# Kernel tuning notes

Measured on AMD Instinct MI355X. Metric: run time of the kernel, lower is better.

The kernel has to match this reference:

```python
import jax, jax.numpy as jnp
import numpy as np

B, L, V, E, D, NH, HD, NL = 4, 2048, 32000, 300, 128, 4, 128, 3
D2 = NH * HD  # 512
W = 3  # ring window size (unfold_size)
EPS = 1e-5


def setup_inputs() -> dict:
    key = jax.random.key(0)
    ks = jax.random.split(key, 16)
    s = 0.02
    w = lambda k, shape: (jax.random.normal(k, shape, jnp.float32) * s)
    inp = {
        "tokens": jax.random.randint(ks[0], (B, L), 0, V),
        "mask": jax.random.randint(ks[1], (B, L), 0, 2).astype(jnp.int32),
        "emb_table": w(ks[2], (V, E)),
        "proj_w": w(ks[3], (D, E)),
        "proj_b": jnp.zeros((D,), jnp.float32),
        "ng": jnp.ones((NL, D), jnp.float32),
        "nb": jnp.zeros((NL, D), jnp.float32),
        "rq_w": w(ks[4], (NL, D2, D)), "rq_b": jnp.zeros((NL, D2), jnp.float32),
        "rk_w": w(ks[5], (NL, D2, D)), "rk_b": jnp.zeros((NL, D2), jnp.float32),
        "rv_w": w(ks[6], (NL, D2, D)), "rv_b": jnp.zeros((NL, D2), jnp.float32),
        "ro_w": w(ks[7], (NL, D, D2)), "ro_b": jnp.zeros((NL, D), jnp.float32),
        "sq_w": w(ks[8], (NL, D2, D)), "sq_b": jnp.zeros((NL, D2), jnp.float32),
        "sk_w": w(ks[9], (NL, D2, D)), "sk_b": jnp.zeros((NL, D2), jnp.float32),
        "sv_w": w(ks[10], (NL, D2, D)), "sv_b": jnp.zeros((NL, D2), jnp.float32),
        "so_w": w(ks[11], (NL, D, D2)), "so_b": jnp.zeros((NL, D), jnp.float32),
    }
    return inp


def _layernorm(x, g, b):
    mu = x.mean(-1, keepdims=True)
    var = x.var(-1, keepdims=True)
    return (x - mu) / jnp.sqrt(var + EPS) * g + b


def reference(tokens, mask, emb_table, proj_w, proj_b, ng, nb,
              rq_w, rq_b, rk_w, rk_b, rv_w, rv_b, ro_w, ro_b,
              sq_w, sq_b, sk_w, sk_b, sv_w, sv_b, so_w, so_b):
    b, l = tokens.shape
    pad = (mask == 0)                                        # [B,L] True at padding
    smask = jnp.concatenate([jnp.zeros((b, 1), bool), pad], axis=1)  # [B,L+1]
    x = emb_table[tokens] @ proj_w.T + proj_b                # [B,L,D]
    nodes = x
    relay = x.mean(axis=1)                                   # [B,D]
    r_embs = x                                               # fixed original embeddings
    scale = 1.0 / np.sqrt(HD).astype(np.float32)
    for i in range(NL):
        nx = _layernorm(nodes, ng[i], nb[i])
        # ----- MSA1: ring (windowed) attention + relay extras -----
        q = (nx @ rq_w[i].T + rq_b[i]).reshape(b, l, NH, HD)
        k = (nx @ rk_w[i].T + rk_b[i]).reshape(b, l, NH, HD)
        v = (nx @ rv_w[i].T + rv_b[i]).reshape(b, l, NH, HD)
        relay_bc = jnp.broadcast_to(relay[:, None, :], (b, l, D))
        ax = jnp.stack([r_embs, relay_bc], axis=2)           # [B,L,2,D]
        ak = (ax @ rk_w[i].T + rk_b[i]).reshape(b, l, 2, NH, HD)
        av = (ax @ rv_w[i].T + rv_b[i]).reshape(b, l, 2, NH, HD)
        kp = jnp.pad(k, ((0, 0), (1, 1), (0, 0), (0, 0)))    # zero pad like F.unfold
        vp = jnp.pad(v, ((0, 0), (1, 1), (0, 0), (0, 0)))
        kw = jnp.stack([kp[:, u:u + l] for u in range(W)], axis=2)  # [B,L,3,NH,HD]
        vw = jnp.stack([vp[:, u:u + l] for u in range(W)], axis=2)
        kall = jnp.concatenate([kw, ak], axis=2)             # [B,L,5,NH,HD]
        vall = jnp.concatenate([vw, av], axis=2)
        scores = jnp.einsum('blnh,blunh->blun', q, kall) * scale
        alphas = jax.nn.softmax(scores, axis=2)
        att = jnp.einsum('blun,blunh->blnh', alphas, vall).reshape(b, l, D2)
        nodes = nodes + jax.nn.leaky_relu(att @ ro_w[i].T + ro_b[i])
        # ----- MSA2: relay (global) attention over [relay; nodes] -----
        y = jnp.concatenate([relay[:, None, :], nodes], axis=1)      # [B,L+1,D]
        sq = (relay @ sq_w[i].T + sq_b[i]).reshape(b, NH, HD)
        sk = (y @ sk_w[i].T + sk_b[i]).reshape(b, l + 1, NH, HD)
        sv = (y @ sv_w[i].T + sv_b[i]).reshape(b, l + 1, NH, HD)
        pre = jnp.einsum('bnh,blnh->bnl', sq, sk) * scale            # [B,NH,L+1]
        pre = jnp.where(smask[:, None, :], -jnp.inf, pre)
        al = jax.nn.softmax(pre, axis=2)
        satt = jnp.einsum('bnl,blnh->bnh', al, sv).reshape(b, D2)
        relay = jax.nn.leaky_relu(satt @ so_w[i].T + so_b[i])
        nodes = jnp.where(pad[:, :, None], 0.0, nodes)
    return relay  # a_v: [B, d_model] (use_attention=False path)
```

## Files before the change

### kernel.cpp

```cpp
#include <hip/hip_runtime.h>
#include <hip/hip_bf16.h>

constexpr int B = 4, L = 2048, E = 300, D = 128, NH = 4, HD = 128, NL = 3, D2 = 512;
constexpr float EPS = 1e-5f;
constexpr float SCALE = 0.08838834764831843f;
constexpr int NCH = 64;

typedef unsigned int uint_t;
typedef unsigned short u16;
typedef short bf16x8 __attribute__((ext_vector_type(8)));
typedef float f32x4 __attribute__((ext_vector_type(4)));

__device__ __forceinline__ u16 f2bf(float f) {
  union { float f; uint_t i; } x; x.f = f;
  uint_t r = x.i + 0x7fffu + ((x.i >> 16) & 1u);
  return (u16)(r >> 16);
}
__device__ __forceinline__ uint_t packbf(float a, float b) {
  return (uint_t)f2bf(a) | ((uint_t)f2bf(b) << 16);
}
__device__ __forceinline__ float2 bf2x2(uint_t u) {
  union { uint_t i; float f; } a, b;
  a.i = (u & 0xffffu) << 16; b.i = u & 0xffff0000u;
  return make_float2(a.f, b.f);
}
struct f8 { float v[8]; };
__device__ __forceinline__ f8 unpack8(uint4 u) {
  f8 r;
  float2 a = bf2x2(u.x); r.v[0] = a.x; r.v[1] = a.y;
  float2 b = bf2x2(u.y); r.v[2] = b.x; r.v[3] = b.y;
  float2 c = bf2x2(u.z); r.v[4] = c.x; r.v[5] = c.y;
  float2 d = bf2x2(u.w); r.v[6] = d.x; r.v[7] = d.y;
  return r;
}

struct WCArgs { const float* s[4]; u16* d[4]; };

struct GDesc { const u16* A; const u16* W; const float* bias; u16* outb; };
struct GArgs { GDesc d[5]; };
struct PArgs {
  int mode;
  const float* rel_in;
  const float* pm; const float* ps; const float* pw;
  const float* uprev; const float* cvprev;
  const float* svw; const float* svb;
  const float* sow; const float* sob;
  float* rel_out;
  const float* rkw; const float* rkb;
  const float* rvw; const float* rvb;
  const float* sqw; const float* sqb;
  const float* skw; const float* skb;
  float* relay_k; float* relay_v;
  float* u; float* cvec;
};
constexpr int NPROJ = 24;

__global__ __launch_bounds__(256) void gemm_qkv(GArgs ga, PArgs pa, int N) {
  int bid = blockIdx.x;
  int t = threadIdx.x;
  if (bid < NPROJ) {
    __shared__ float rel[D];
    __shared__ float sql2[2][HD];
    __shared__ float credp[4];
    __shared__ float wsum2[NH][D];
    __shared__ float satts[D2];
    __shared__ float ecs2[256];
    int b = bid / 6, j = bid % 6;
    int wv = t >> 6, lane = t & 63;
    if (pa.mode) {
      if (t < D) rel[t] = pa.rel_in[(size_t)b * D + t];
      __syncthreads();
      float2 uu = ((const float2*)(pa.uprev + ((size_t)b * NH + wv) * D))[lane];
      float2 rr = ((const float2*)rel)[lane];
      float pdot = uu.x * rr.x + uu.y * rr.y;
#pragma unroll
      for (int o = 1; o < 64; o <<= 1) pdot += __shfl_xor(pdot, o, 64);
      float s0 = pdot + pa.cvprev[b * NH + wv];
      int bn = b * NH + wv;
      float pmv = pa.pm[bn * NCH + lane];
      float m = fmaxf(pmv, s0);
#pragma unroll
      for (int o = 1; o < 64; o <<= 1) m = fmaxf(m, __shfl_xor(m, o, 64));
      float ec = expf(pmv - m);
      ecs2[wv * 64 + lane] = ec;
      float sc = pa.ps[bn * NCH + lane] * ec;
#pragma unroll
      for (int o = 1; o < 64; o <<= 1) sc += __shfl_xor(sc, o, 64);
      float e0 = expf(s0 - m);
      float invS = 1.0f / (e0 + sc);
      float2 a;
      a.x = e0 * rel[lane * 2]; a.y = e0 * rel[lane * 2 + 1];
      const float* pwb = pa.pw + (size_t)bn * NCH * D;
#pragma unroll 8
      for (int c = 0; c < NCH; c++) {
        float2 pw2 = ((const float2*)(pwb + (size_t)c * D))[lane];
        float e = ecs2[wv * 64 + c];
        a.x += e * pw2.x; a.y += e * pw2.y;
      }
      wsum2[wv][lane * 2] = a.x * invS;
      wsum2[wv][lane * 2 + 1] = a.y * invS;
      __syncthreads();
#pragma unroll
      for (int pp = 0; pp < 2; pp++) {
        int nh = pp * 256 + t, n = nh >> 7;
        float acc = pa.svb[nh];
        const float4* wp = (const float4*)(pa.svw + (size_t)nh * D);
        const float4* wl = (const float4*)wsum2[n];
#pragma unroll 8
        for (int dd = 0; dd < D / 4; dd++) {
          float4 x = wl[dd], y = wp[dd];
          acc += x.x * y.x + x.y * y.y + x.z * y.z + x.w * y.w;
        }
        satts[nh] = acc;
      }
      __syncthreads();
      {
        int part = t >> 7, col = t & 127;
        float acc = 0.f;
        const float4* wp = (const float4*)(pa.sow + (size_t)col * D2 + part * 256);
        const float4* a4 = (const float4*)(satts + part * 256);
#pragma unroll 8
        for (int jj = 0; jj < 64; jj++) {
          float4 x = a4[jj], y = wp[jj];
          acc += x.x * y.x + x.y * y.y + x.z * y.z + x.w * y.w;
        }
        ecs2[part * 128 + col] = acc;
      }
      __syncthreads();
      if (t < D) {
        float av = pa.sob[t] + ecs2[t] + ecs2[128 + t];
        av = (av > 0.f) ? av : 0.01f * av;
        rel[t] = av;
        pa.rel_out[(size_t)b * D + t] = av;
      }
      __syncthreads();
    } else {
      if (t < D) rel[t] = pa.rel_in[(size_t)b * D + t];
      __syncthreads();
    }
    const float4* r4 = (const float4*)rel;
    if (j < 4) {
      int which = j >> 1;
      int n = (j & 1) * 256 + t;
      const float* W = which ? pa.rvw : pa.rkw;
      float acc = (which ? pa.rvb : pa.rkb)[n];
      const float4* w4 = (const float4*)(W + (size_t)n * D);
#pragma unroll 8
      for (int i = 0; i < D / 4; i++) {
        float4 w = w4[i], r = r4[i];
        acc += w.x * r.x + w.y * r.y + w.z * r.z + w.w * r.w;
      }
      (which ? pa.relay_v : pa.relay_k)[(size_t)b * D2 + n] = acc;
    } else {
      int hh = t >> 7, th = t & 127;
      int n = (j - 4) * 2 + hh;
      int nh = n * HD + th;
      float acc = pa.sqb[nh];
      const float4* w4 = (const float4*)(pa.sqw + (size_t)nh * D);
#pragma unroll 8
      for (int i = 0; i < D / 4; i++) {
        float4 w = w4[i], r = r4[i];
        acc += w.x * r.x + w.y * r.y + w.z * r.z + w.w * r.w;
      }
      sql2[hh][th] = acc;
      __syncthreads();
      float cp = acc * pa.skb[nh];
#pragma unroll
      for (int o = 1; o < 64; o <<= 1) cp += __shfl_xor(cp, o, 64);
      if ((t & 63) == 0) credp[t >> 6] = cp;
      float a0 = 0.f, a1 = 0.f, a2 = 0.f, a3 = 0.f;
      const float* wp = pa.skw + (size_t)(n * HD) * D + th;
      for (int hx = 0; hx < HD; hx += 4) {
        a0 += sql2[hh][hx] * wp[(size_t)hx * D];
        a1 += sql2[hh][hx + 1] * wp[(size_t)(hx + 1) * D];
        a2 += sql2[hh][hx + 2] * wp[(size_t)(hx + 2) * D];
        a3 += sql2[hh][hx + 3] * wp[(size_t)(hx + 3) * D];
      }
      pa.u[((size_t)b * NH + n) * D + th] = (a0 + a1 + a2 + a3) * SCALE;
      __syncthreads();
      if (th == 0) pa.cvec[b * NH + n] = (credp[2 * hh] + credp[2 * hh + 1]) * SCALE;
    }
    return;
  }
  __shared__ u16 As[128][136];
  __shared__ u16 Ws[128][136];
  int g = bid - NPROJ;
  int grp = g >> 8;
  int bm = (g & 255) >> 2, bn = g & 3;
  const int di0 = grp ? 3 : 0;
  const int ntens = grp ? 2 : 3;
  const int rowA = bm * 128, rowW = bn * 128;

  const int r = t >> 1, c0 = (t & 1) * 64;
  const int wid = t >> 6;
  const int wm = (wid & 1) * 64, wn = (wid >> 1) * 64;
  const int lr = t & 15, quad = (t >> 4) & 3;

  {
    const u16* Arow = ga.d[di0].A + (size_t)(rowA + r) * 128;
    uint4 av_[8];
#pragma unroll
    for (int i = 0; i < 8; i++) av_[i] = *(const uint4*)(Arow + c0 + i * 8);
#pragma unroll
    for (int i = 0; i < 8; i++) *(uint4*)&As[r][c0 + i * 8] = av_[i];
  }
  for (int ti = 0; ti < ntens; ti++) {
    GDesc d = ga.d[di0 + ti];
    {
      const u16* Wrow = d.W + (size_t)(rowW + r) * 128;
      uint4 wv_[8];
#pragma unroll
      for (int i = 0; i < 8; i++) wv_[i] = *(const uint4*)(Wrow + c0 + i * 8);
#pragma unroll
      for (int i = 0; i < 8; i++) *(uint4*)&Ws[r][c0 + i * 8] = wv_[i];
    }
    __syncthreads();
    f32x4 acc[4][4];
#pragma unroll
    for (int i = 0; i < 4; i++)
#pragma unroll
      for (int j = 0; j < 4; j++)
        acc[i][j] = (f32x4){0.f, 0.f, 0.f, 0.f};
#pragma unroll
    for (int ks = 0; ks < 4; ks++) {
      bf16x8 af[4], bfr[4];
#pragma unroll
      for (int mt = 0; mt < 4; mt++)
        af[mt] = *(const bf16x8*)&As[wm + mt * 16 + lr][ks * 32 + quad * 8];
#pragma unroll
      for (int nt = 0; nt < 4; nt++)
        bfr[nt] = *(const bf16x8*)&Ws[wn + nt * 16 + lr][ks * 32 + quad * 8];
#pragma unroll
      for (int mt = 0; mt < 4; mt++)
#pragma unroll
        for (int nt = 0; nt < 4; nt++)
          acc[mt][nt] = __builtin_amdgcn_mfma_f32_16x16x32_bf16(af[mt], bfr[nt], acc[mt][nt], 0, 0, 0);
    }
    __syncthreads();
#pragma unroll
    for (int nt = 0; nt < 4; nt++) {
      int colL = wn + nt * 16 + lr;
      float bv = d.bias[rowW + colL];
#pragma unroll
      for (int mt = 0; mt < 4; mt++) {
#pragma unroll
        for (int rr = 0; rr < 4; rr++) {
          int rowL = wm + mt * 16 + quad * 4 + rr;
          Ws[rowL][colL] = f2bf(acc[mt][nt][rr] + bv);
        }
      }
    }
    __syncthreads();
#pragma unroll
    for (int rep = 0; rep < 8; rep++) {
      int lin = rep * 256 + t;
      int rowL = lin >> 4, colL = (lin & 15) * 8;
      uint4 v = *(const uint4*)&Ws[rowL][colL];
      *(uint4*)&d.outb[(size_t)(rowA + rowL) * N + rowW + colL] = v;
    }
    __syncthreads();
  }
}

__global__ __launch_bounds__(256) void gemm_embed_ln(
    WCArgs wa,
    const float* __restrict__ emb, const float* __restrict__ W,
    const float* __restrict__ bias, const int* __restrict__ gather,
    const float* __restrict__ lng, const float* __restrict__ lnb,
    float* __restrict__ nodes, u16* __restrict__ xb, u16* __restrict__ nxb,
    float* __restrict__ relay) {
  int bid = blockIdx.x;
  int t = threadIdx.x;
  if (bid >= 128) {
    int cb = bid - 128;
    int ti = cb / 192, xi = cb - ti * 192;
    const float* s = wa.s[ti]; u16* dd = wa.d[ti];
    int i = (xi * 256 + t) * 4;
    float4 f = *(const float4*)(s + i);
    *(uint2*)(dd + i) = make_uint2(packbf(f.x, f.y), packbf(f.z, f.w));
    return;
  }
  __shared__ u16 As[64][72];
  __shared__ u16 Ws[128][72];
  __shared__ float C[64][132];
  __shared__ float gb[2][D];
  __shared__ float lmu[64], lrs[64];
  int bm = bid;
  const int rowA0 = bm * 64;

  f32x4 acc[2][4];
#pragma unroll
  for (int i = 0; i < 2; i++)
#pragma unroll
    for (int j = 0; j < 4; j++)
      acc[i][j] = (f32x4){0.f, 0.f, 0.f, 0.f};

  const int wid = t >> 6;
  const int wm = (wid & 1) * 32, wn = (wid >> 1) * 64;
  const int lr = t & 15, quad = (t >> 4) & 3;
  const int ra = t >> 2, ca = (t & 3) * 16;
  const int rw = t >> 1, cw = (t & 1) * 32;

  if (t < D) { gb[0][t] = lng[t]; gb[1][t] = lnb[t]; }

  const float* Arow = emb + (size_t)gather[rowA0 + ra] * E;
  const float* Wrow = W + (size_t)rw * E;

  for (int kt = 0; kt < E; kt += 64) {
    __syncthreads();
    bool full = (kt + 64 <= E);
#pragma unroll
    for (int ch = 0; ch < 4; ch++) {
      int c = kt + ca + ch * 4;
      float4 fa;
      if (full) fa = *(const float4*)(Arow + c);
      else {
        fa.x = (c + 0 < E) ? Arow[c + 0] : 0.f;
        fa.y = (c + 1 < E) ? Arow[c + 1] : 0.f;
        fa.z = (c + 2 < E) ? Arow[c + 2] : 0.f;
        fa.w = (c + 3 < E) ? Arow[c + 3] : 0.f;
      }
      *(uint2*)&As[ra][ca + ch * 4] = make_uint2(packbf(fa.x, fa.y), packbf(fa.z, fa.w));
    }
#pragma unroll
    for (int ch = 0; ch < 8; ch++) {
      int c = kt + cw + ch * 4;
      float4 fw;
      if (full) fw = *(const float4*)(Wrow + c);
      else {
        fw.x = (c + 0 < E) ? Wrow[c + 0] : 0.f;
        fw.y = (c + 1 < E) ? Wrow[c + 1] : 0.f;
        fw.z = (c + 2 < E) ? Wrow[c + 2] : 0.f;
        fw.w = (c + 3 < E) ? Wrow[c + 3] : 0.f;
      }
      *(uint2*)&Ws[rw][cw + ch * 4] = make_uint2(packbf(fw.x, fw.y), packbf(fw.z, fw.w));
    }
    __syncthreads();
#pragma unroll
    for (int ks = 0; ks < 2; ks++) {
      bf16x8 af[2], bfr[4];
#pragma unroll
      for (int mt = 0; mt < 2; mt++)
        af[mt] = *(const bf16x8*)&As[wm + mt * 16 + lr][ks * 32 + quad * 8];
#pragma unroll
      for (int nt = 0; nt < 4; nt++)
        bfr[nt] = *(const bf16x8*)&Ws[wn + nt * 16 + lr][ks * 32 + quad * 8];
#pragma unroll
      for (int mt = 0; mt < 2; mt++)
#pragma unroll
        for (int nt = 0; nt < 4; nt++)
          acc[mt][nt] = __builtin_amdgcn_mfma_f32_16x16x32_bf16(af[mt], bfr[nt], acc[mt][nt], 0, 0, 0);
    }
  }
#pragma unroll
  for (int nt = 0; nt < 4; nt++) {
    int col = wn + nt * 16 + lr;
    float bv = bias[col];
#pragma unroll
    for (int mt = 0; mt < 2; mt++) {
#pragma unroll
      for (int rr = 0; rr < 4; rr++) {
        int row = wm + mt * 16 + quad * 4 + rr;
        C[row][col] = acc[mt][nt][rr] + bv;
      }
    }
  }
  __syncthreads();
  if (t < 64) {
    float s = 0.f, s2 = 0.f;
#pragma unroll 16
    for (int j = 0; j < D; j++) { float v = C[t][j]; s += v; s2 += v * v; }
    float mu = s * (1.0f / D);
    float var = s2 * (1.0f / D) - mu * mu;
    lmu[t] = mu; lrs[t] = rsqrtf(var + EPS);
  }
  __syncthreads();
#pragma unroll
  for (int rep = 0; rep < 8; rep++) {
    int lin = rep * 1024 + t * 4;
    int row = lin >> 7, col = lin & 127;
    float4 v = *(const float4*)&C[row][col];
    size_t g = (size_t)(rowA0 + row) * D + col;
    *(float4*)&nodes[g] = v;
    *(uint2*)&xb[g] = make_uint2(packbf(v.x, v.y), packbf(v.z, v.w));
    float mu = lmu[row], rs = lrs[row];
    float o0 = (v.x - mu) * rs * gb[0][col] + gb[1][col];
    float o1 = (v.y - mu) * rs * gb[0][col + 1] + gb[1][col + 1];
    float o2 = (v.z - mu) * rs * gb[0][col + 2] + gb[1][col + 2];
    float o3 = (v.w - mu) * rs * gb[0][col + 3] + gb[1][col + 3];
    *(uint2*)&nxb[g] = make_uint2(packbf(o0, o1), packbf(o2, o3));
  }
  if (t < D) {
    int b = rowA0 >> 11;
    float s = 0.f;
#pragma unroll 16
    for (int r2 = 0; r2 < 64; r2++) s += C[r2][t];
    atomicAdd(&relay[b * D + t], s * (1.0f / L));
  }
}

__global__ __launch_bounds__(512) void attn_ro_ln(
    const u16* __restrict__ q, const u16* __restrict__ k, const u16* __restrict__ v,
    const u16* __restrict__ akr, const u16* __restrict__ avr,
    const float* __restrict__ rkvec, const float* __restrict__ rvvec,
    const u16* __restrict__ W,
    const float* __restrict__ bias,
    const int* __restrict__ mask,
    const float* __restrict__ lng, const float* __restrict__ lnb,
    const float* __restrict__ uvec, const float* __restrict__ cvec,
    float* __restrict__ nodes, u16* __restrict__ nxb,
    float* __restrict__ pm, float* __restrict__ ps, float* __restrict__ pw,
    int do_ln) {
  __shared__ u16 att[32][520];
  __shared__ u16 Ws[128][136];
  __shared__ float C[32][132];
  __shared__ float gb[2][D];
  __shared__ float lmu[32], lrs[32];
  __shared__ float usv[NH][D];
  __shared__ float cv2[NH];
  __shared__ float scs[NH][32];
  __shared__ float esr[NH][32];
  int t = threadIdx.x;
  int bm = blockIdx.x;
  const int rowA0 = bm * 32;
  const int b4 = rowA0 >> 11;
  const int chunk = (rowA0 >> 5) & 63;
  const int wid = t >> 6, lane = t & 63;

  if (do_ln && t < D) { gb[0][t] = lng[t]; gb[1][t] = lnb[t]; }
  usv[t >> 7][t & 127] = uvec[(size_t)b4 * NH * D + t];
  if (t < NH) cv2[t] = cvec[b4 * NH + t];

  {
    size_t rb = (size_t)b4 * D2 + lane * 8;
    float4 rk0 = *(const float4*)(rkvec + rb), rk1 = *(const float4*)(rkvec + rb + 4);
    float4 rv0 = *(const float4*)(rvvec + rb), rv1 = *(const float4*)(rvvec + rb + 4);
    f8 krel, vrel;
    krel.v[0] = rk0.x; krel.v[1] = rk0.y; krel.v[2] = rk0.z; krel.v[3] = rk0.w;
    krel.v[4] = rk1.x; krel.v[5] = rk1.y; krel.v[6] = rk1.z; krel.v[7] = rk1.w;
    vrel.v[0] = rv0.x; vrel.v[1] = rv0.y; vrel.v[2] = rv0.z; vrel.v[3] = rv0.w;
    vrel.v[4] = rv1.x; vrel.v[5] = rv1.y; vrel.v[6] = rv1.z; vrel.v[7] = rv1.w;
#pragma unroll
    for (int i = 0; i < 4; i++) {
      int rr_ = wid * 4 + i;
      int gr = rowA0 + rr_;
      int l = gr & (L - 1);
      size_t rowoff = (size_t)gr * D2 + lane * 8;
      uint4 qd = *(const uint4*)(q + rowoff);
      uint4 kd[4], vd[4];
#pragma unroll
      for (int u2 = 0; u2 < 3; u2++) {
        int ll = l + u2 - 1;
        bool ok = (ll >= 0 && ll < L);
        size_t off = rowoff + (size_t)(u2 - 1) * (size_t)D2;
        if (ok) { kd[u2] = *(const uint4*)(k + off); vd[u2] = *(const uint4*)(v + off); }
        else { kd[u2] = make_uint4(0, 0, 0, 0); vd[u2] = make_uint4(0, 0, 0, 0); }
      }
      kd[3] = *(const uint4*)(akr + rowoff);
      vd[3] = *(const uint4*)(avr + rowoff);
      f8 qf = unpack8(qd);
      f8 kf[5], vf[5];
#pragma unroll
      for (int u2 = 0; u2 < 4; u2++) { kf[u2] = unpack8(kd[u2]); vf[u2] = unpack8(vd[u2]); }
      kf[4] = krel; vf[4] = vrel;
      float s[5];
#pragma unroll
      for (int u2 = 0; u2 < 5; u2++) {
        float p = 0.f;
#pragma unroll
        for (int j = 0; j < 8; j++) p += qf.v[j] * kf[u2].v[j];
#pragma unroll
        for (int o = 1; o < 16; o <<= 1) p += __shfl_xor(p, o, 64);
        s[u2] = p * SCALE;
      }
      float m = s[0];
#pragma unroll
      for (int u2 = 1; u2 < 5; u2++) m = fmaxf(m, s[u2]);
      float e[5], sum = 0.f;
#pragma unroll
      for (int u2 = 0; u2 < 5; u2++) { e[u2] = expf(s[u2] - m); sum += e[u2]; }
      float inv = 1.0f / sum;
      float o8[8];
#pragma unroll
      for (int j = 0; j < 8; j++) {
        float a = 0.f;
#pragma unroll
        for (int u2 = 0; u2 < 5; u2++) a += e[u2] * vf[u2].v[j];
        o8[j] = a * inv;
      }
      uint4 od;
      od.x = packbf(o8[0], o8[1]); od.y = packbf(o8[2], o8[3]);
      od.z = packbf(o8[4], o8[5]); od.w = packbf(o8[6], o8[7]);
      *(uint4*)&att[rr_][lane * 8] = od;
    }
  }
  __syncthreads();

  f32x4 acc[2];
  acc[0] = (f32x4){0.f, 0.f, 0.f, 0.f};
  acc[1] = (f32x4){0.f, 0.f, 0.f, 0.f};
  const int wm = (wid & 1) * 16, wn = (wid >> 1) * 32;
  const int lr = t & 15, quad = (t >> 4) & 3;
  const int rw = t >> 2, cw = (t & 3) * 32;
  const u16* Wrow = W + (size_t)rw * 512;
  for (int kt = 0; kt < 512; kt += 128) {
    uint4 w0 = *(const uint4*)(Wrow + kt + cw);
    uint4 w1 = *(const uint4*)(Wrow + kt + cw + 8);
    uint4 w2 = *(const uint4*)(Wrow + kt + cw + 16);
    uint4 w3 = *(const uint4*)(Wrow + kt + cw + 24);
    __syncthreads();
    *(uint4*)&Ws[rw][cw] = w0; *(uint4*)&Ws[rw][cw + 8] = w1;
    *(uint4*)&Ws[rw][cw + 16] = w2; *(uint4*)&Ws[rw][cw + 24] = w3;
    __syncthreads();
#pragma unroll
    for (int ks = 0; ks < 4; ks++) {
      bf16x8 af = *(const bf16x8*)&att[wm + lr][kt + ks * 32 + quad * 8];
#pragma unroll
      for (int nt = 0; nt < 2; nt++) {
        bf16x8 bfr = *(const bf16x8*)&Ws[wn + nt * 16 + lr][ks * 32 + quad * 8];
        acc[nt] = __builtin_amdgcn_mfma_f32_16x16x32_bf16(af, bfr, acc[nt], 0, 0, 0);
      }
    }
  }
  __syncthreads();
#pragma unroll
  for (int nt = 0; nt < 2; nt++) {
    int col = wn + nt * 16 + lr;
    float bv = bias[col];
#pragma unroll
    for (int rr = 0; rr < 4; rr++) {
      int row = wm + quad * 4 + rr;
      float vv = acc[nt][rr] + bv;
      vv = (vv > 0.f) ? vv : 0.01f * vv;
      vv += nodes[(size_t)(rowA0 + row) * D + col];
      if (mask[rowA0 + row] == 0) vv = 0.f;
      C[row][col] = vv;
    }
  }
  __syncthreads();
  if (t < 32) {
    float s = 0.f, s2 = 0.f;
#pragma unroll 16
    for (int j = 0; j < D; j++) { float vv = C[t][j]; s += vv; s2 += vv * vv; }
    float mu = s * (1.0f / D);
    float var = s2 * (1.0f / D) - mu * mu;
    lmu[t] = mu; lrs[t] = rsqrtf(var + EPS);
  }
  __syncthreads();
#pragma unroll
  for (int rep = 0; rep < 2; rep++) {
    int lin = rep * 2048 + t * 4;
    int row = lin >> 7, col = lin & 127;
    float4 vv = *(const float4*)&C[row][col];
    size_t g = (size_t)(rowA0 + row) * D + col;
    *(float4*)&nodes[g] = vv;
    if (do_ln) {
      float mu = lmu[row], rs = lrs[row];
      float o0 = (vv.x - mu) * rs * gb[0][col] + gb[1][col];
      float o1 = (vv.y - mu) * rs * gb[0][col + 1] + gb[1][col + 1];
      float o2 = (vv.z - mu) * rs * gb[0][col + 2] + gb[1][col + 2];
      float o3 = (vv.w - mu) * rs * gb[0][col + 3] + gb[1][col + 3];
      *(uint2*)&nxb[g] = make_uint2(packbf(o0, o1), packbf(o2, o3));
    }
  }
  if (wid < 4) {
    int n = wid;
    int bn = b4 * NH + n;
    const float2* un = (const float2*)usv[n];
    float2 uv2 = un[lane];
    for (int r2 = 0; r2 < 32; r2++) {
      float2 cc = ((const float2*)&C[r2][0])[lane];
      float p = uv2.x * cc.x + uv2.y * cc.y;
#pragma unroll
      for (int o = 1; o < 64; o <<= 1) p += __shfl_xor(p, o, 64);
      if (lane == 0) {
        float s = p + cv2[n];
        if (mask[rowA0 + r2] == 0) s = -1e30f;
        scs[n][r2] = s;
      }
    }
    float m = -1e30f;
    for (int r2 = 0; r2 < 32; r2++) m = fmaxf(m, scs[n][r2]);
    if (lane < 32) esr[n][lane] = expf(scs[n][lane] - m);
    float sum = 0.f;
    for (int r2 = 0; r2 < 32; r2++) sum += esr[n][r2];
    if (lane == 0) { pm[bn * NCH + chunk] = m; ps[bn * NCH + chunk] = sum; }
    float a0 = 0.f, a1 = 0.f;
    for (int r2 = 0; r2 < 32; r2++) {
      float e = esr[n][r2];
      float2 cc = ((const float2*)&C[r2][0])[lane];
      a0 += e * cc.x; a1 += e * cc.y;
    }
    float* pwp = pw + ((size_t)bn * NCH + chunk) * D + 2 * lane;
    pwp[0] = a0; pwp[1] = a1;
  }
}

__global__ __launch_bounds__(512) void relay_combine(
    const float* __restrict__ pm, const float* __restrict__ ps,
    const float* __restrict__ pw,
    const float* __restrict__ relay_entry,
    const float* __restrict__ uvec_in, const float* __restrict__ cvec_in,
    const float* __restrict__ svw, const float* __restrict__ svb,
    const float* __restrict__ sow, const float* __restrict__ sob,
    float* __restrict__ relay_out) {
  __shared__ float rel0[D];
  __shared__ float wpart[8];
  __shared__ float ecs[NH][NCH];
  __shared__ float wsum[NH][D];
  __shared__ float satts[D2];
  __shared__ float rred[4][D];
  int b = blockIdx.x, t = threadIdx.x;
  int n = t >> 7, h = t & 127;
  int w = t >> 6, lane = t & 63;
  if (t < D) rel0[t] = relay_entry[(size_t)b * D + t];
  __syncthreads();
  float p = uvec_in[((size_t)b * NH + n) * D + h] * rel0[h];
#pragma unroll
  for (int o = 1; o < 64; o <<= 1) p += __shfl_xor(p, o, 64);
  if (lane == 0) wpart[w] = p;
  __syncthreads();
  float s0 = wpart[2 * n] + wpart[2 * n + 1] + cvec_in[b * NH + n];
  int c = h & 63;
  float pmv = pm[(b * NH + n) * NCH + c];
  float m = fmaxf(pmv, s0);
#pragma unroll
  for (int o = 1; o < 64; o <<= 1) m = fmaxf(m, __shfl_xor(m, o, 64));
  float ec = expf(pmv - m);
  if (h < 64) ecs[n][h] = ec;
  float sc = ps[(b * NH + n) * NCH + c] * ec;
#pragma unroll
  for (int o = 1; o < 64; o <<= 1) sc += __shfl_xor(sc, o, 64);
  float e0 = expf(s0 - m);
  float invS = 1.0f / (e0 + sc);
  __syncthreads();
  float acc = e0 * rel0[h];
  const float* pwp = pw + ((size_t)(b * NH + n) * NCH) * D + h;
#pragma unroll 8
  for (int cc = 0; cc < NCH; cc++) acc += ecs[n][cc] * pwp[(size_t)cc * D];
  wsum[n][h] = acc * invS;
  __syncthreads();
  {
    float a = svb[t];
    const float4* wp = (const float4*)(svw + (size_t)t * D);
    const float4* wl = (const float4*)wsum[n];
#pragma unroll 8
    for (int dd = 0; dd < D / 4; dd++) {
      float4 x = wl[dd], y = wp[dd];
      a += x.x * y.x + x.y * y.y + x.z * y.z + x.w * y.w;
    }
    satts[t] = a;
  }
  __syncthreads();
  {
    int part = t >> 7, col = t & 127;
    float a = 0.f;
    const float4* wp = (const float4*)(sow + (size_t)col * D2 + part * 128);
    const float4* a4 = (const float4*)(satts + part * 128);
#pragma unroll 8
    for (int jj = 0; jj < 32; jj++) {
      float4 x = a4[jj], y = wp[jj];
      a += x.x * y.x + x.y * y.y + x.z * y.z + x.w * y.w;
    }
    rred[part][col] = a;
  }
  __syncthreads();
  if (t < D) {
    float a = sob[t] + rred[0][t] + rred[1][t] + rred[2][t] + rred[3][t];
    a = (a > 0.f) ? a : 0.01f * a;
    relay_out[(size_t)b * D + t] = a;
  }
}

extern "C" void kernel_launch(void* const* d_in, const int* in_sizes, int n_in,
                              void* d_out, int out_size, void* d_ws, size_t ws_size,
                              hipStream_t stream) {
  const int* tokens = (const int*)d_in[0];
  const int* mask = (const int*)d_in[1];
  const float* emb = (const float*)d_in[2];
  const float* proj_w = (const float*)d_in[3];
  const float* proj_b = (const float*)d_in[4];
  const float* ng = (const float*)d_in[5];
  const float* nb = (const float*)d_in[6];
  const float* rq_w = (const float*)d_in[7], * rq_b = (const float*)d_in[8];
  const float* rk_w = (const float*)d_in[9], * rk_b = (const float*)d_in[10];
  const float* rv_w = (const float*)d_in[11], * rv_b = (const float*)d_in[12];
  const float* ro_w = (const float*)d_in[13], * ro_b = (const float*)d_in[14];
  const float* sq_w = (const float*)d_in[15], * sq_b = (const float*)d_in[16];
  const float* sk_w = (const float*)d_in[17], * sk_b = (const float*)d_in[18];
  const float* sv_w = (const float*)d_in[19], * sv_b = (const float*)d_in[20];
  const float* so_w = (const float*)d_in[21], * so_b = (const float*)d_in[22];

  const size_t BLD = (size_t)B * L * D;
  const size_t BLD4 = (size_t)B * L * D2;
  const size_t WTEN = (size_t)NL * D * D2;

  float* fp = (float*)d_ws;
  float* nodes = fp;                    fp += BLD;
  float* rbuf0 = fp;                    fp += B * D;
  float* rbuf1 = fp;                    fp += B * D;
  float* relay_k = fp;                  fp += B * D2;
  float* relay_v = fp;                  fp += B * D2;
  float* uv0 = fp;                      fp += B * NH * D;
  float* uv1 = fp;                      fp += B * NH * D;
  float* cv0 = fp;                      fp += B * NH;
  float* cv1 = fp;                      fp += B * NH;
  float* pm = fp;                       fp += B * NH * NCH;
  float* ps = fp;                       fp += B * NH * NCH;
  float* pw = fp;                       fp += (size_t)B * NH * NCH * D;
  u16* up = (u16*)fp;
  u16* xb = up;                         up += BLD;
  u16* nxb = up;                        up += BLD;
  u16* qb = up;                         up += BLD4;
  u16* kb = up;                         up += BLD4;
  u16* vb = up;                         up += BLD4;
  u16* akb = up;                        up += BLD4;
  u16* avb = up;                        up += BLD4;
  u16* wb = up;
  u16* wrq = wb, * wrk = wb + WTEN, * wrv = wb + 2 * WTEN, * wro = wb + 3 * WTEN;

  float* uv[2] = {uv0, uv1};
  float* cv[2] = {cv0, cv1};

  hipMemsetAsync(rbuf0, 0, B * D * sizeof(float), stream);

  {
    WCArgs wa;
    wa.s[0] = rq_w; wa.s[1] = rk_w; wa.s[2] = rv_w; wa.s[3] = ro_w;
    wa.d[0] = wrq; wa.d[1] = wrk; wa.d[2] = wrv; wa.d[3] = wro;
    gemm_embed_ln<<<128 + 768, 256, 0, stream>>>(wa, emb, proj_w, proj_b, tokens,
                                                 ng, nb, nodes, xb, nxb, rbuf0);
  }

  float* rel_in_l[3] = {rbuf0, rbuf0, rbuf1};
  float* rel_out_l[3] = {nullptr, rbuf1, rbuf0};

  for (int i = 0; i < NL; i++) {
    const size_t wo = (size_t)i * D * D2;
    const float* rqbi = rq_b + (size_t)i * D2;
    const float* rkbi = rk_b + (size_t)i * D2;
    const float* rvbi = rv_b + (size_t)i * D2;
    const float* robi = ro_b + (size_t)i * D;
    const int e = i & 1, ep = (i > 0) ? ((i - 1) & 1) : 0;
    const int last = (i == NL - 1);

    {
      GArgs ga = {};
      ga.d[0] = {nxb, wrq + wo, rqbi, qb};
      ga.d[1] = {nxb, wrk + wo, rkbi, kb};
      ga.d[2] = {nxb, wrv + wo, rvbi, vb};
      ga.d[3] = {xb,  wrk + wo, rkbi, akb};
      ga.d[4] = {xb,  wrv + wo, rvbi, avb};
      PArgs pa;
      pa.mode = (i == 0) ? 0 : 1;
      pa.rel_in = rel_in_l[i];
      pa.pm = pm; pa.ps = ps; pa.pw = pw;
      pa.uprev = uv[ep]; pa.cvprev = cv[ep];
      const size_t wprev = (size_t)(i > 0 ? i - 1 : 0) * D * D2;
      pa.svw = sv_w + wprev; pa.svb = sv_b + (size_t)(i > 0 ? i - 1 : 0) * D2;
      pa.sow = so_w + wprev; pa.sob = so_b + (size_t)(i > 0 ? i - 1 : 0) * D;
      pa.rel_out = rel_out_l[i];
      pa.rkw = rk_w + wo; pa.rkb = rkbi;
      pa.rvw = rv_w + wo; pa.rvb = rvbi;
      pa.sqw = sq_w + wo; pa.sqb = sq_b + (size_t)i * D2;
      pa.skw = sk_w + wo; pa.skb = sk_b + (size_t)i * D2;
      pa.relay_k = relay_k; pa.relay_v = relay_v; pa.u = uv[e]; pa.cvec = cv[e];
      gemm_qkv<<<512 + NPROJ, 256, 0, stream>>>(ga, pa, D2);
    }
    attn_ro_ln<<<256, 512, 0, stream>>>(
        qb, kb, vb, akb, avb, relay_k, relay_v,
        wro + wo, robi, mask,
        last ? nullptr : ng + (i + 1) * D, last ? nullptr : nb + (i + 1) * D,
        uv[e], cv[e], nodes, nxb, pm, ps, pw, last ? 0 : 1);
  }
  const size_t w2 = (size_t)(NL - 1) * D * D2;
  relay_combine<<<B, 512, 0, stream>>>(pm, ps, pw, rbuf0,
                                       uv[(NL - 1) & 1], cv[(NL - 1) & 1],
                                       sv_w + w2, sv_b + (size_t)(NL - 1) * D2,
                                       so_w + w2, so_b + (size_t)(NL - 1) * D,
                                       (float*)d_out);
}
```

Before: 320.6 us.

## Halve attn_ro_ln row tile to 16 and double relay partial chunks

The fused ring-attention/output-projection/layernorm kernel now processes 16 rows per block instead of 32, launching 512 blocks rather than 256 so more CUs stay busy. Each wave now owns a single 16x16 MFMA output tile. The number of relay-softmax partial chunks per sequence doubles to 128, so the combine code in gemm_qkv and relay_combine reads two partials per lane. The price is more partial (m, s, w) records to write and reduce, and each block reloads the full Wo tile for half as many rows. A __syncthreads is also added before shared ecs2 is reused, which guards against a race now that the buffer is larger and shared across waves.

```diff
diff --git a/kernel.cpp b/kernel.cpp
--- a/kernel.cpp
+++ b/kernel.cpp
@@ -4,7 +4,7 @@
 constexpr int B = 4, L = 2048, E = 300, D = 128, NH = 4, HD = 128, NL = 3, D2 = 512;
 constexpr float EPS = 1e-5f;
 constexpr float SCALE = 0.08838834764831843f;
-constexpr int NCH = 64;
+constexpr int NCH = 128;
 
 typedef unsigned int uint_t;
 typedef unsigned short u16;
@@ -64,7 +64,7 @@
     __shared__ float credp[4];
     __shared__ float wsum2[NH][D];
     __shared__ float satts[D2];
-    __shared__ float ecs2[256];
+    __shared__ float ecs2[NH * NCH];
     int b = bid / 6, j = bid % 6;
     int wv = t >> 6, lane = t & 63;
     if (pa.mode) {
@@ -77,13 +77,15 @@
       for (int o = 1; o < 64; o <<= 1) pdot += __shfl_xor(pdot, o, 64);
       float s0 = pdot + pa.cvprev[b * NH + wv];
       int bn = b * NH + wv;
-      float pmv = pa.pm[bn * NCH + lane];
-      float m = fmaxf(pmv, s0);
+      float pmv0 = pa.pm[bn * NCH + lane];
+      float pmv1 = pa.pm[bn * NCH + 64 + lane];
+      float m = fmaxf(fmaxf(pmv0, pmv1), s0);
 #pragma unroll
       for (int o = 1; o < 64; o <<= 1) m = fmaxf(m, __shfl_xor(m, o, 64));
-      float ec = expf(pmv - m);
-      ecs2[wv * 64 + lane] = ec;
-      float sc = pa.ps[bn * NCH + lane] * ec;
+      float ec0 = expf(pmv0 - m), ec1 = expf(pmv1 - m);
+      ecs2[wv * NCH + lane] = ec0;
+      ecs2[wv * NCH + 64 + lane] = ec1;
+      float sc = pa.ps[bn * NCH + lane] * ec0 + pa.ps[bn * NCH + 64 + lane] * ec1;
 #pragma unroll
       for (int o = 1; o < 64; o <<= 1) sc += __shfl_xor(sc, o, 64);
       float e0 = expf(s0 - m);
@@ -94,7 +96,7 @@
 #pragma unroll 8
       for (int c = 0; c < NCH; c++) {
         float2 pw2 = ((const float2*)(pwb + (size_t)c * D))[lane];
-        float e = ecs2[wv * 64 + c];
+        float e = ecs2[wv * NCH + c];
         a.x += e * pw2.x; a.y += e * pw2.y;
       }
       wsum2[wv][lane * 2] = a.x * invS;
@@ -124,6 +126,7 @@
           float4 x = a4[jj], y = wp[jj];
           acc += x.x * y.x + x.y * y.y + x.z * y.z + x.w * y.w;
         }
+        __syncthreads();
         ecs2[part * 128 + col] = acc;
       }
       __syncthreads();
@@ -411,20 +414,20 @@
     float* __restrict__ nodes, u16* __restrict__ nxb,
     float* __restrict__ pm, float* __restrict__ ps, float* __restrict__ pw,
     int do_ln) {
-  __shared__ u16 att[32][520];
+  __shared__ u16 att[16][520];
   __shared__ u16 Ws[128][136];
-  __shared__ float C[32][132];
+  __shared__ float C[16][132];
   __shared__ float gb[2][D];
-  __shared__ float lmu[32], lrs[32];
+  __shared__ float lmu[16], lrs[16];
   __shared__ float usv[NH][D];
   __shared__ float cv2[NH];
-  __shared__ float scs[NH][32];
-  __shared__ float esr[NH][32];
+  __shared__ float scs[NH][16];
+  __shared__ float esr[NH][16];
   int t = threadIdx.x;
   int bm = blockIdx.x;
-  const int rowA0 = bm * 32;
+  const int rowA0 = bm * 16;
   const int b4 = rowA0 >> 11;
-  const int chunk = (rowA0 >> 5) & 63;
+  const int chunk = (rowA0 >> 4) & (NCH - 1);
   const int wid = t >> 6, lane = t & 63;
 
   if (do_ln && t < D) { gb[0][t] = lng[t]; gb[1][t] = lnb[t]; }
@@ -441,8 +444,8 @@
     vrel.v[0] = rv0.x; vrel.v[1] = rv0.y; vrel.v[2] = rv0.z; vrel.v[3] = rv0.w;
     vrel.v[4] = rv1.x; vrel.v[5] = rv1.y; vrel.v[6] = rv1.z; vrel.v[7] = rv1.w;
 #pragma unroll
-    for (int i = 0; i < 4; i++) {
-      int rr_ = wid * 4 + i;
+    for (int i = 0; i < 2; i++) {
+      int rr_ = wid * 2 + i;
       int gr = rowA0 + rr_;
       int l = gr & (L - 1);
       size_t rowoff = (size_t)gr * D2 + lane * 8;
@@ -496,10 +499,9 @@
   }
   __syncthreads();
 
-  f32x4 acc[2];
-  acc[0] = (f32x4){0.f, 0.f, 0.f, 0.f};
-  acc[1] = (f32x4){0.f, 0.f, 0.f, 0.f};
-  const int wm = (wid & 1) * 16, wn = (wid >> 1) * 32;
+  f32x4 acc;
+  acc = (f32x4){0.f, 0.f, 0.f, 0.f};
+  const int wn = wid * 16;
   const int lr = t & 15, quad = (t >> 4) & 3;
   const int rw = t >> 2, cw = (t & 3) * 32;
   const u16* Wrow = W + (size_t)rw * 512;
@@ -514,23 +516,19 @@
     __syncthreads();
 #pragma unroll
     for (int ks = 0; ks < 4; ks++) {
-      bf16x8 af = *(const bf16x8*)&att[wm + lr][kt + ks * 32 + quad * 8];
-#pragma unroll
-      for (int nt = 0; nt < 2; nt++) {
-        bf16x8 bfr = *(const bf16x8*)&Ws[wn + nt * 16 + lr][ks * 32 + quad * 8];
-        acc[nt] = __builtin_amdgcn_mfma_f32_16x16x32_bf16(af, bfr, acc[nt], 0, 0, 0);
-      }
-    }
-  }
-  __syncthreads();
-#pragma unroll
-  for (int nt = 0; nt < 2; nt++) {
-    int col = wn + nt * 16 + lr;
+      bf16x8 af = *(const bf16x8*)&att[lr][kt + ks * 32 + quad * 8];
+      bf16x8 bfr = *(const bf16x8*)&Ws[wn + lr][ks * 32 + quad * 8];
+      acc = __builtin_amdgcn_mfma_f32_16x16x32_bf16(af, bfr, acc, 0, 0, 0);
+    }
+  }
+  __syncthreads();
+  {
+    int col = wn + lr;
     float bv = bias[col];
 #pragma unroll
     for (int rr = 0; rr < 4; rr++) {
-      int row = wm + quad * 4 + rr;
-      float vv = acc[nt][rr] + bv;
+      int row = quad * 4 + rr;
+      float vv = acc[rr] + bv;
       vv = (vv > 0.f) ? vv : 0.01f * vv;
       vv += nodes[(size_t)(rowA0 + row) * D + col];
       if (mask[rowA0 + row] == 0) vv = 0.f;
@@ -538,7 +536,7 @@
     }
   }
   __syncthreads();
-  if (t < 32) {
+  if (t < 16) {
     float s = 0.f, s2 = 0.f;
 #pragma unroll 16
     for (int j = 0; j < D; j++) { float vv = C[t][j]; s += vv; s2 += vv * vv; }
@@ -547,9 +545,8 @@
     lmu[t] = mu; lrs[t] = rsqrtf(var + EPS);
   }
   __syncthreads();
-#pragma unroll
-  for (int rep = 0; rep < 2; rep++) {
-    int lin = rep * 2048 + t * 4;
+  {
+    int lin = t * 4;
     int row = lin >> 7, col = lin & 127;
     float4 vv = *(const float4*)&C[row][col];
     size_t g = (size_t)(rowA0 + row) * D + col;
@@ -568,7 +565,7 @@
     int bn = b4 * NH + n;
     const float2* un = (const float2*)usv[n];
     float2 uv2 = un[lane];
-    for (int r2 = 0; r2 < 32; r2++) {
+    for (int r2 = 0; r2 < 16; r2++) {
       float2 cc = ((const float2*)&C[r2][0])[lane];
       float p = uv2.x * cc.x + uv2.y * cc.y;
 #pragma unroll
@@ -580,13 +577,13 @@
       }
     }
     float m = -1e30f;
-    for (int r2 = 0; r2 < 32; r2++) m = fmaxf(m, scs[n][r2]);
-    if (lane < 32) esr[n][lane] = expf(scs[n][lane] - m);
+    for (int r2 = 0; r2 < 16; r2++) m = fmaxf(m, scs[n][r2]);
+    if (lane < 16) esr[n][lane] = expf(scs[n][lane] - m);
     float sum = 0.f;
-    for (int r2 = 0; r2 < 32; r2++) sum += esr[n][r2];
+    for (int r2 = 0; r2 < 16; r2++) sum += esr[n][r2];
     if (lane == 0) { pm[bn * NCH + chunk] = m; ps[bn * NCH + chunk] = sum; }
     float a0 = 0.f, a1 = 0.f;
-    for (int r2 = 0; r2 < 32; r2++) {
+    for (int r2 = 0; r2 < 16; r2++) {
       float e = esr[n][r2];
       float2 cc = ((const float2*)&C[r2][0])[lane];
       a0 += e * cc.x; a1 += e * cc.y;
@@ -622,13 +619,14 @@
   __syncthreads();
   float s0 = wpart[2 * n] + wpart[2 * n + 1] + cvec_in[b * NH + n];
   int c = h & 63;
-  float pmv = pm[(b * NH + n) * NCH + c];
-  float m = fmaxf(pmv, s0);
+  float pmv0 = pm[(b * NH + n) * NCH + c];
+  float pmv1 = pm[(b * NH + n) * NCH + 64 + c];
+  float m = fmaxf(fmaxf(pmv0, pmv1), s0);
 #pragma unroll
   for (int o = 1; o < 64; o <<= 1) m = fmaxf(m, __shfl_xor(m, o, 64));
-  float ec = expf(pmv - m);
-  if (h < 64) ecs[n][h] = ec;
-  float sc = ps[(b * NH + n) * NCH + c] * ec;
+  float ec0 = expf(pmv0 - m), ec1 = expf(pmv1 - m);
+  if (h < 64) { ecs[n][h] = ec0; ecs[n][64 + h] = ec1; }
+  float sc = ps[(b * NH + n) * NCH + c] * ec0 + ps[(b * NH + n) * NCH + 64 + c] * ec1;
 #pragma unroll
   for (int o = 1; o < 64; o <<= 1) sc += __shfl_xor(sc, o, 64);
   float e0 = expf(s0 - m);
@@ -767,7 +765,7 @@
       pa.relay_k = relay_k; pa.relay_v = relay_v; pa.u = uv[e]; pa.cvec = cv[e];
       gemm_qkv<<<512 + NPROJ, 256, 0, stream>>>(ga, pa, D2);
     }
-    attn_ro_ln<<<256, 512, 0, stream>>>(
+    attn_ro_ln<<<512, 512, 0, stream>>>(
         qb, kb, vb, akb, avb, relay_k, relay_v,
         wro + wo, robi, mask,
         last ? nullptr : ng + (i + 1) * D, last ? nullptr : nb + (i + 1) * D,
```

Result: faster. 310.1 us (median of 2 runs) (-3.3%).
